# Performance work log

Measured on AMD Instinct MI355X. Metric: run time of the kernel, lower is better.

The kernel has to match this reference:

```python
import jax, jax.numpy as jnp
import numpy as np

D_MODEL, D_LOW, NUM_BINS = 512, 64, 39
DIST_MIN, DIST_MAX = 2.0, 22.0
BIN_WIDTH = (DIST_MAX - DIST_MIN) / (NUM_BINS - 1)
LN_EPS = 1e-5


def setup_inputs() -> dict:
    key = jax.random.key(0)
    ks = jax.random.split(key, 10)
    B, N = 2, 768
    h_res = jax.random.normal(ks[0], (B, N, D_MODEL), dtype=jnp.float32)
    # scale coords so pairwise distances span the [2, 22] bin range
    x_true = jax.random.normal(ks[1], (B, N, 3), dtype=jnp.float32) * 5.0
    token_pad_mask = jnp.ones((B, N), dtype=jnp.float32)
    s = 1.0 / np.sqrt(D_MODEL)
    return {
        "h_res": h_res,
        "x_true": x_true,
        "token_pad_mask": token_pad_mask,
        "ln_w": jnp.ones((D_MODEL,), jnp.float32),
        "ln_b": jnp.zeros((D_MODEL,), jnp.float32),
        "wu_w": jax.random.normal(ks[2], (D_LOW, D_MODEL), jnp.float32) * s,
        "wu_b": jnp.zeros((D_LOW,), jnp.float32),
        "wv_w": jax.random.normal(ks[3], (D_LOW, D_MODEL), jnp.float32) * s,
        "wv_b": jnp.zeros((D_LOW,), jnp.float32),
        "wb_w": jax.random.normal(ks[4], (NUM_BINS, D_LOW), jnp.float32) * (1.0 / np.sqrt(D_LOW)),
        "wb_b": jnp.zeros((NUM_BINS,), jnp.float32),
    }


def _layernorm(x, w, b):
    mu = jnp.mean(x, axis=-1, keepdims=True)
    var = jnp.mean(jnp.square(x - mu), axis=-1, keepdims=True)
    return (x - mu) * jax.lax.rsqrt(var + LN_EPS) * w + b


def reference(h_res, x_true, token_pad_mask, ln_w, ln_b, wu_w, wu_b, wv_w, wv_b, wb_w, wb_b):
    B, N, _ = h_res.shape
    # pairwise distances -> target bins (trunc-to-int then clamp, as torch .long())
    diff = x_true[:, :, None, :] - x_true[:, None, :, :]          # [B,N,N,3]
    d_true = jnp.sqrt(jnp.sum(diff * diff, axis=-1))               # [B,N,N]
    target = jnp.clip(((d_true - DIST_MIN) / BIN_WIDTH).astype(jnp.int32), 0, NUM_BINS - 1)

    h = _layernorm(h_res, ln_w, ln_b)
    U = h @ wu_w.T + wu_b                                          # [B,N,d_low]
    V = h @ wv_w.T + wv_b                                          # [B,N,d_low]
    # logits[b,i,j,k] = sum_c U[b,i,c] V[b,j,c] Wb[k,c] + bb[k]
    logits = jnp.einsum("bic,bjc,kc->bijk", U, V, wb_w) + wb_b     # [B,N,N,K]
    logp = jax.nn.log_softmax(logits, axis=-1)
    ce = -jnp.take_along_axis(logp, target[..., None], axis=-1)[..., 0]  # [B,N,N]

    mask = (token_pad_mask[:, :, None] * token_pad_mask[:, None, :]) > 0  # [B,N,N] bool
    counts = jnp.sum(mask, axis=(1, 2))                            # [B]
    per_sample = jnp.sum(jnp.where(mask, ce, 0.0), axis=(1, 2)) / jnp.maximum(counts, 1)
    valid = counts > 0
    total_count = jnp.sum(valid)
    loss = jnp.sum(jnp.where(valid, per_sample, 0.0)) / jnp.maximum(total_count, 1)
    return loss
```

## Files before the change

### kernel.cpp

```cpp
#include <hip/hip_runtime.h>
#include <hip/hip_bf16.h>
#include <math.h>

#define D_MODEL 512
#define D_LOW   64
#define NBINS   39
#define LOG2E   1.4426950408889634f
#define LN2     0.6931471805599453f

typedef __attribute__((ext_vector_type(8))) short short8;
typedef __attribute__((ext_vector_type(4))) float floatx4;

__global__ __launch_bounds__(256) void lnp_kernel(
    const float* __restrict__ h_res,
    const float* __restrict__ ln_w, const float* __restrict__ ln_b,
    const float* __restrict__ wu_w, const float* __restrict__ wu_b,
    const float* __restrict__ wv_w, const float* __restrict__ wv_b,
    float* __restrict__ U, __hip_bfloat16* __restrict__ Vbf, int N) {
  __shared__ short abuf[16 * 512];
  __shared__ float sred[4][2][16];
  const int tid = threadIdx.x;
  const int wv = tid >> 6, lane = tid & 63;
  const int q = lane >> 4, ln16 = lane & 15;
  const int row0 = blockIdx.x * 16;
  const int og = blockIdx.y;

  float sum = 0.f, ssq = 0.f;
  #pragma unroll
  for (int k2 = 0; k2 < 4; ++k2) {
    const int kc = wv * 4 + k2;
    const float* hp = h_res + (size_t)(row0 + ln16) * D_MODEL + kc * 32 + q * 8;
    const floatx4 x0 = *reinterpret_cast<const floatx4*>(hp);
    const floatx4 x1 = *reinterpret_cast<const floatx4*>(hp + 4);
    short8 a;
    #pragma unroll
    for (int e = 0; e < 4; ++e) {
      sum += x0[e]; ssq += x0[e] * x0[e];
      const __hip_bfloat16 hb = __float2bfloat16(x0[e]);
      a[e] = *reinterpret_cast<const short*>(&hb);
    }
    #pragma unroll
    for (int e = 0; e < 4; ++e) {
      sum += x1[e]; ssq += x1[e] * x1[e];
      const __hip_bfloat16 hb = __float2bfloat16(x1[e]);
      a[4 + e] = *reinterpret_cast<const short*>(&hb);
    }
    *reinterpret_cast<short8*>(&abuf[kc * 512 + q * 128 + ln16 * 8]) = a;
  }
  sum += __shfl_xor(sum, 16); sum += __shfl_xor(sum, 32);
  ssq += __shfl_xor(ssq, 16); ssq += __shfl_xor(ssq, 32);
  if (lane < 16) { sred[wv][0][ln16] = sum; sred[wv][1][ln16] = ssq; }

  const int oloc = wv * 16 + ln16;
  const float scale = og ? 1.0f : LOG2E;
  const float* wrow = (og ? wv_w : wu_w) + (size_t)oloc * D_MODEL;
  short8 bfrag[16];
  float ws = 0.f, sb = 0.f;
  #pragma unroll
  for (int kc = 0; kc < 16; ++kc) {
    const int c0 = kc * 32 + q * 8;
    const floatx4 w0 = *reinterpret_cast<const floatx4*>(wrow + c0);
    const floatx4 w1 = *reinterpret_cast<const floatx4*>(wrow + c0 + 4);
    const floatx4 lw0 = *reinterpret_cast<const floatx4*>(ln_w + c0);
    const floatx4 lw1 = *reinterpret_cast<const floatx4*>(ln_w + c0 + 4);
    const floatx4 lb0 = *reinterpret_cast<const floatx4*>(ln_b + c0);
    const floatx4 lb1 = *reinterpret_cast<const floatx4*>(ln_b + c0 + 4);
    short8 f;
    #pragma unroll
    for (int e = 0; e < 4; ++e) {
      const float t0 = w0[e] * lw0[e] * scale;
      const __hip_bfloat16 h0 = __float2bfloat16(t0);
      f[e] = *reinterpret_cast<const short*>(&h0);
      ws += __bfloat162float(h0);
      sb += w0[e] * lb0[e];

      const float t1 = w1[e] * lw1[e] * scale;
      const __hip_bfloat16 h1 = __float2bfloat16(t1);
      f[4 + e] = *reinterpret_cast<const short*>(&h1);
      ws += __bfloat162float(h1);
      sb += w1[e] * lb1[e];
    }
    bfrag[kc] = f;
  }
  ws += __shfl_xor(ws, 16); ws += __shfl_xor(ws, 32);
  sb += __shfl_xor(sb, 16); sb += __shfl_xor(sb, 32);
  const float bb = scale * ((og ? wv_b[oloc] : wu_b[oloc]) + sb);

  __syncthreads();

  float mu_r[4], rs_r[4];
  #pragma unroll
  for (int r = 0; r < 4; ++r) {
    const int row = q * 4 + r;
    float s = 0.f, s2 = 0.f;
    #pragma unroll
    for (int w = 0; w < 4; ++w) { s += sred[w][0][row]; s2 += sred[w][1][row]; }
    const float mu  = s * (1.0f / (float)D_MODEL);
    const float var = s2 * (1.0f / (float)D_MODEL) - mu * mu;
    mu_r[r] = mu;
    rs_r[r] = rsqrtf(var + 1e-5f);
  }

  floatx4 acc = (floatx4){0.f, 0.f, 0.f, 0.f};
  #pragma unroll
  for (int kc = 0; kc < 16; ++kc) {
    const short8 afr = *reinterpret_cast<const short8*>(
        &abuf[kc * 512 + q * 128 + ln16 * 8]);
    acc = __builtin_amdgcn_mfma_f32_16x16x32_bf16(afr, bfrag[kc], acc, 0, 0, 0);
  }

  #pragma unroll
  for (int r = 0; r < 4; ++r) {
    const int rowg = row0 + q * 4 + r;
    const float val = rs_r[r] * acc[r] - mu_r[r] * rs_r[r] * ws + bb;
    if (og == 0) {
      U[(size_t)rowg * D_LOW + oloc] = val;
    } else {
      Vbf[(size_t)rowg * D_LOW + oloc] = __float2bfloat16(val);
    }
  }
}

__global__ __launch_bounds__(256, 4) void pair_kernel(
    const float* __restrict__ U, const __hip_bfloat16* __restrict__ Vbf,
    const float* __restrict__ wb_w, const float* __restrict__ wb_b,
    const float* __restrict__ x_true, const float* __restrict__ pmask,
    float* __restrict__ part, int N) {
  __shared__ short wsh[6 * 64 * 8];
  __shared__ float rbuf[8];
  const int i    = blockIdx.x;
  const int b    = blockIdx.y >> 2;
  const int qtr  = blockIdx.y & 3;
  const int tid  = threadIdx.x;
  const int wave = tid >> 6, lane = tid & 63;
  const int q = lane >> 4, ln16 = lane & 15;
  const int rowi = b * N + i;
  const int jbase = qtr * (N >> 2) + wave * (N >> 4);
  const int q4 = q * 4;

  const short* Vp = reinterpret_cast<const short*>(Vbf) + (size_t)b * N * D_LOW;
  short8 v[3][2];
  #pragma unroll
  for (int tl = 0; tl < 3; ++tl) {
    const size_t jr = jbase + tl * 16 + ln16;
    v[tl][0] = *reinterpret_cast<const short8*>(Vp + jr * D_LOW + q * 8);
    v[tl][1] = *reinterpret_cast<const short8*>(Vp + jr * D_LOW + 32 + q * 8);
  }

  for (int slot = tid; slot < 384; slot += 256) {
    const int fidx = slot >> 6, l = slot & 63;
    const int t = fidx >> 1, s = fidx & 1;
    const int lq = l >> 4, l16 = l & 15;
    const int n = t * 16 + l16;
    short8 fr = (short8){0, 0, 0, 0, 0, 0, 0, 0};
    if (n < NBINS) {
      const float* up = U + (size_t)rowi * D_LOW + s * 32 + lq * 8;
      const float* wr = wb_w + (size_t)n * D_LOW + s * 32 + lq * 8;
      const floatx4 u0 = *reinterpret_cast<const floatx4*>(up);
      const floatx4 u1 = *reinterpret_cast<const floatx4*>(up + 4);
      const floatx4 w0 = *reinterpret_cast<const floatx4*>(wr);
      const floatx4 w1 = *reinterpret_cast<const floatx4*>(wr + 4);
      #pragma unroll
      for (int e = 0; e < 4; ++e) {
        const __hip_bfloat16 h0 = __float2bfloat16(u0[e] * w0[e]);
        const __hip_bfloat16 h1 = __float2bfloat16(u1[e] * w1[e]);
        fr[e]     = *reinterpret_cast<const short*>(&h0);
        fr[4 + e] = *reinterpret_cast<const short*>(&h1);
      }
    }
    *reinterpret_cast<short8*>(&wsh[slot * 8]) = fr;
  }

  const float xi0 = x_true[rowi * 3 + 0];
  const float xi1 = x_true[rowi * 3 + 1];
  const float xi2 = x_true[rowi * 3 + 2];
  const float pmi = pmask[rowi];
  const float BW  = (22.0f - 2.0f) / 38.0f;
  int tbv[3];
  #pragma unroll
  for (int tl = 0; tl < 3; ++tl) {
    const int rowj = b * N + jbase + tl * 16 + ln16;
    const float dx = xi0 - x_true[rowj * 3 + 0];
    const float dy = xi1 - x_true[rowj * 3 + 1];
    const float dz = xi2 - x_true[rowj * 3 + 2];
    const float d  = sqrtf(dx * dx + dy * dy + dz * dz);
    int tb = (int)((d - 2.0f) / BW);
    tb = tb < 0 ? 0 : (tb > NBINS - 1 ? NBINS - 1 : tb);
    tbv[tl] = (pmi * pmask[rowj] > 0.f) ? tb : -1;
  }

  floatx4 bias_init[3];
  #pragma unroll
  for (int t = 0; t < 3; ++t)
    #pragma unroll
    for (int r = 0; r < 4; ++r) {
      const int bin = t * 16 + q * 4 + r;
      bias_init[t][r] = (bin < NBINS) ? LOG2E * wb_b[bin] : -INFINITY;
    }

  __syncthreads();
  short8 wfrag[3][2];
  #pragma unroll
  for (int t = 0; t < 3; ++t)
    #pragma unroll
    for (int s = 0; s < 2; ++s)
      wfrag[t][s] = *reinterpret_cast<const short8*>(
          &wsh[((t * 2 + s) * 64 + lane) * 8]);

  floatx4 f[3][3];
  #pragma unroll
  for (int tl = 0; tl < 3; ++tl)
    #pragma unroll
    for (int t = 0; t < 3; ++t) {
      floatx4 a = bias_init[t];
      a = __builtin_amdgcn_mfma_f32_16x16x32_bf16(wfrag[t][0], v[tl][0], a, 0, 0, 0);
      a = __builtin_amdgcn_mfma_f32_16x16x32_bf16(wfrag[t][1], v[tl][1], a, 0, 0, 0);
      f[tl][t] = a;
    }

  float sp[3], ltv[3];
  #pragma unroll
  for (int tl = 0; tl < 3; ++tl) {
    const int tbq = tbv[tl] - q4;
    float s0 = 0.f, s1 = 0.f, s2 = 0.f, s3 = 0.f, lt = 0.f;
    #pragma unroll
    for (int t = 0; t < 3; ++t) {
      const floatx4 fv = f[tl][t];
      s0 += __builtin_amdgcn_exp2f(fv[0]);
      s1 += __builtin_amdgcn_exp2f(fv[1]);
      s2 += __builtin_amdgcn_exp2f(fv[2]);
      s3 += __builtin_amdgcn_exp2f(fv[3]);
      lt += (tbq == t * 16 + 0) ? fv[0] : 0.f;
      lt += (tbq == t * 16 + 1) ? fv[1] : 0.f;
      lt += (tbq == t * 16 + 2) ? fv[2] : 0.f;
      lt += (tbq == t * 16 + 3) ? fv[3] : 0.f;
    }
    sp[tl] = (s0 + s1) + (s2 + s3);
    ltv[tl] = lt;
  }

  #pragma unroll
  for (int tl = 0; tl < 3; ++tl) sp[tl] += __shfl_xor(sp[tl], 16);
  #pragma unroll
  for (int tl = 0; tl < 3; ++tl) sp[tl] += __shfl_xor(sp[tl], 32);

  float ce_sum = 0.f, cnt_sum = 0.f;
  #pragma unroll
  for (int tl = 0; tl < 3; ++tl) {
    const float ok = (tbv[tl] >= 0) ? 1.f : 0.f;
    ce_sum  += ok * LN2 * (__builtin_amdgcn_logf(sp[tl]) - 4.0f * ltv[tl]);
    cnt_sum += ok;
  }

  #pragma unroll
  for (int off = 32; off; off >>= 1) {
    ce_sum  += __shfl_xor(ce_sum, off);
    cnt_sum += __shfl_xor(cnt_sum, off);
  }
  if (lane == 0) { rbuf[wave] = ce_sum; rbuf[4 + wave] = cnt_sum; }
  __syncthreads();
  if (tid == 0) {
    const size_t slot = ((size_t)blockIdx.y * N + blockIdx.x) * 2;
    part[slot + 0] = rbuf[0] + rbuf[1] + rbuf[2] + rbuf[3];
    part[slot + 1] = rbuf[4] + rbuf[5] + rbuf[6] + rbuf[7];
  }
}

__global__ __launch_bounds__(256) void finalize_kernel(
    const float* __restrict__ part, float* __restrict__ out, int N, int B) {
  __shared__ float red[8];
  const int tid = threadIdx.x, wave = tid >> 6, lane = tid & 63;
  float loss = 0.f, vcount = 0.f;
  const int nper = 4 * N;
  for (int b = 0; b < B; ++b) {
    float ce = 0.f, cnt = 0.f;
    for (int e = tid; e < nper; e += 256) {
      const size_t base = ((size_t)b * nper + e) * 2;
      ce  += part[base + 0];
      cnt += part[base + 1];
    }
    #pragma unroll
    for (int off = 32; off; off >>= 1) {
      ce  += __shfl_xor(ce, off);
      cnt += __shfl_xor(cnt, off);
    }
    if (lane == 0) { red[wave] = ce; red[4 + wave] = cnt; }
    __syncthreads();
    if (tid == 0) {
      const float s = red[0] + red[1] + red[2] + red[3];
      const float c = red[4] + red[5] + red[6] + red[7];
      if (c > 0.f) { loss += s / fmaxf(c, 1.f); vcount += 1.f; }
    }
    __syncthreads();
  }
  if (tid == 0) out[0] = (vcount > 0.f) ? loss / vcount : 0.f;
}

extern "C" void kernel_launch(void* const* d_in, const int* in_sizes, int n_in,
                              void* d_out, int out_size, void* d_ws, size_t ws_size,
                              hipStream_t stream) {
  const float* h_res  = (const float*)d_in[0];
  const float* x_true = (const float*)d_in[1];
  const float* pmask  = (const float*)d_in[2];
  const float* ln_w   = (const float*)d_in[3];
  const float* ln_b   = (const float*)d_in[4];
  const float* wu_w   = (const float*)d_in[5];
  const float* wu_b   = (const float*)d_in[6];
  const float* wv_w   = (const float*)d_in[7];
  const float* wv_b   = (const float*)d_in[8];
  const float* wb_w   = (const float*)d_in[9];
  const float* wb_b   = (const float*)d_in[10];

  const int B  = 2;
  const int N  = in_sizes[2] / B;
  const int BN = B * N;

  float* U = (float*)d_ws;
  __hip_bfloat16* Vbf = (__hip_bfloat16*)(U + (size_t)BN * D_LOW);
  float* part = (float*)(Vbf + (size_t)BN * D_LOW);

  lnp_kernel<<<dim3(BN / 16, 2), 256, 0, stream>>>(
      h_res, ln_w, ln_b, wu_w, wu_b, wv_w, wv_b, U, Vbf, N);
  pair_kernel<<<dim3(N, 4 * B), 256, 0, stream>>>(
      U, Vbf, wb_w, wb_b, x_true, pmask, part, N);
  finalize_kernel<<<1, 256, 0, stream>>>(part, (float*)d_out, N, B);
}
```

Before: 134.3 us.

## Process four query rows per pair block with 512 threads, reusing V fragments

Reorganizes the pair kernel so each 512-thread block handles four i rows across all N columns (8 waves, 96 columns each) instead of one i row over a quarter of the columns. V fragments loaded into registers are reused across four i rows, and the block count drops from 6144 to 384. The aim is to amortize V loads, weight-fragment setup and launch overhead. In exchange, register pressure rises (6x2 V fragments plus a 4x6 target table), occupancy hints are dropped, and the grid has fewer blocks, which may underfill the GPU.

```diff
diff --git a/kernel.cpp b/kernel.cpp
--- a/kernel.cpp
+++ b/kernel.cpp
@@ -121,41 +121,41 @@
   }
 }
 
-__global__ __launch_bounds__(256, 4) void pair_kernel(
+__global__ __launch_bounds__(512) void pair_kernel(
     const float* __restrict__ U, const __hip_bfloat16* __restrict__ Vbf,
     const float* __restrict__ wb_w, const float* __restrict__ wb_b,
     const float* __restrict__ x_true, const float* __restrict__ pmask,
     float* __restrict__ part, int N) {
-  __shared__ short wsh[6 * 64 * 8];
-  __shared__ float rbuf[8];
-  const int i    = blockIdx.x;
-  const int b    = blockIdx.y >> 2;
-  const int qtr  = blockIdx.y & 3;
-  const int tid  = threadIdx.x;
-  const int wave = tid >> 6, lane = tid & 63;
+  __shared__ short wsh[4 * 6 * 64 * 8];
+  __shared__ float rbuf[16];
+  const int tid = threadIdx.x;
+  const int wv = tid >> 6, lane = tid & 63;
   const int q = lane >> 4, ln16 = lane & 15;
-  const int rowi = b * N + i;
-  const int jbase = qtr * (N >> 2) + wave * (N >> 4);
+  const int i0 = blockIdx.x * 4;
+  const int b  = (i0 >= N) ? 1 : 0;
+  const int jbase = wv * (N >> 3);
   const int q4 = q * 4;
 
   const short* Vp = reinterpret_cast<const short*>(Vbf) + (size_t)b * N * D_LOW;
-  short8 v[3][2];
-  #pragma unroll
-  for (int tl = 0; tl < 3; ++tl) {
+  short8 v[6][2];
+  #pragma unroll
+  for (int tl = 0; tl < 6; ++tl) {
     const size_t jr = jbase + tl * 16 + ln16;
     v[tl][0] = *reinterpret_cast<const short8*>(Vp + jr * D_LOW + q * 8);
     v[tl][1] = *reinterpret_cast<const short8*>(Vp + jr * D_LOW + 32 + q * 8);
   }
 
-  for (int slot = tid; slot < 384; slot += 256) {
-    const int fidx = slot >> 6, l = slot & 63;
-    const int t = fidx >> 1, s = fidx & 1;
+  for (int s = tid; s < 1536; s += 512) {
+    const int ii = s / 384;
+    const int rem = s - ii * 384;
+    const int fidx = rem >> 6, l = rem & 63;
+    const int t = fidx >> 1, ss = fidx & 1;
     const int lq = l >> 4, l16 = l & 15;
     const int n = t * 16 + l16;
     short8 fr = (short8){0, 0, 0, 0, 0, 0, 0, 0};
     if (n < NBINS) {
-      const float* up = U + (size_t)rowi * D_LOW + s * 32 + lq * 8;
-      const float* wr = wb_w + (size_t)n * D_LOW + s * 32 + lq * 8;
+      const float* up = U + (size_t)(i0 + ii) * D_LOW + ss * 32 + lq * 8;
+      const float* wr = wb_w + (size_t)n * D_LOW + ss * 32 + lq * 8;
       const floatx4 u0 = *reinterpret_cast<const floatx4*>(up);
       const floatx4 u1 = *reinterpret_cast<const floatx4*>(up + 4);
       const floatx4 w0 = *reinterpret_cast<const floatx4*>(wr);
@@ -168,25 +168,37 @@
         fr[4 + e] = *reinterpret_cast<const short*>(&h1);
       }
     }
-    *reinterpret_cast<short8*>(&wsh[slot * 8]) = fr;
-  }
-
-  const float xi0 = x_true[rowi * 3 + 0];
-  const float xi1 = x_true[rowi * 3 + 1];
-  const float xi2 = x_true[rowi * 3 + 2];
-  const float pmi = pmask[rowi];
-  const float BW  = (22.0f - 2.0f) / 38.0f;
-  int tbv[3];
-  #pragma unroll
-  for (int tl = 0; tl < 3; ++tl) {
+    *reinterpret_cast<short8*>(&wsh[s * 8]) = fr;
+  }
+
+  float xi0v[4], xi1v[4], xi2v[4], pmiv[4];
+  #pragma unroll
+  for (int ii = 0; ii < 4; ++ii) {
+    const int rowi = i0 + ii;
+    xi0v[ii] = x_true[rowi * 3 + 0];
+    xi1v[ii] = x_true[rowi * 3 + 1];
+    xi2v[ii] = x_true[rowi * 3 + 2];
+    pmiv[ii] = pmask[rowi];
+  }
+  const float BW = (22.0f - 2.0f) / 38.0f;
+  int tb[4][6];
+  #pragma unroll
+  for (int tl = 0; tl < 6; ++tl) {
     const int rowj = b * N + jbase + tl * 16 + ln16;
-    const float dx = xi0 - x_true[rowj * 3 + 0];
-    const float dy = xi1 - x_true[rowj * 3 + 1];
-    const float dz = xi2 - x_true[rowj * 3 + 2];
-    const float d  = sqrtf(dx * dx + dy * dy + dz * dz);
-    int tb = (int)((d - 2.0f) / BW);
-    tb = tb < 0 ? 0 : (tb > NBINS - 1 ? NBINS - 1 : tb);
-    tbv[tl] = (pmi * pmask[rowj] > 0.f) ? tb : -1;
+    const float xj0 = x_true[rowj * 3 + 0];
+    const float xj1 = x_true[rowj * 3 + 1];
+    const float xj2 = x_true[rowj * 3 + 2];
+    const float pmj = pmask[rowj];
+    #pragma unroll
+    for (int ii = 0; ii < 4; ++ii) {
+      const float dx = xi0v[ii] - xj0;
+      const float dy = xi1v[ii] - xj1;
+      const float dz = xi2v[ii] - xj2;
+      const float d  = sqrtf(dx * dx + dy * dy + dz * dz);
+      int t = (int)((d - 2.0f) / BW);
+      t = t < 0 ? 0 : (t > NBINS - 1 ? NBINS - 1 : t);
+      tb[ii][tl] = (pmiv[ii] * pmj > 0.f) ? t : -1;
+    }
   }
 
   floatx4 bias_init[3];
@@ -199,57 +211,50 @@
     }
 
   __syncthreads();
-  short8 wfrag[3][2];
-  #pragma unroll
-  for (int t = 0; t < 3; ++t)
-    #pragma unroll
-    for (int s = 0; s < 2; ++s)
-      wfrag[t][s] = *reinterpret_cast<const short8*>(
-          &wsh[((t * 2 + s) * 64 + lane) * 8]);
-
-  floatx4 f[3][3];
-  #pragma unroll
-  for (int tl = 0; tl < 3; ++tl)
-    #pragma unroll
-    for (int t = 0; t < 3; ++t) {
-      floatx4 a = bias_init[t];
-      a = __builtin_amdgcn_mfma_f32_16x16x32_bf16(wfrag[t][0], v[tl][0], a, 0, 0, 0);
-      a = __builtin_amdgcn_mfma_f32_16x16x32_bf16(wfrag[t][1], v[tl][1], a, 0, 0, 0);
-      f[tl][t] = a;
-    }
-
-  float sp[3], ltv[3];
-  #pragma unroll
-  for (int tl = 0; tl < 3; ++tl) {
-    const int tbq = tbv[tl] - q4;
-    float s0 = 0.f, s1 = 0.f, s2 = 0.f, s3 = 0.f, lt = 0.f;
-    #pragma unroll
-    for (int t = 0; t < 3; ++t) {
-      const floatx4 fv = f[tl][t];
-      s0 += __builtin_amdgcn_exp2f(fv[0]);
-      s1 += __builtin_amdgcn_exp2f(fv[1]);
-      s2 += __builtin_amdgcn_exp2f(fv[2]);
-      s3 += __builtin_amdgcn_exp2f(fv[3]);
-      lt += (tbq == t * 16 + 0) ? fv[0] : 0.f;
-      lt += (tbq == t * 16 + 1) ? fv[1] : 0.f;
-      lt += (tbq == t * 16 + 2) ? fv[2] : 0.f;
-      lt += (tbq == t * 16 + 3) ? fv[3] : 0.f;
-    }
-    sp[tl] = (s0 + s1) + (s2 + s3);
-    ltv[tl] = lt;
-  }
-
-  #pragma unroll
-  for (int tl = 0; tl < 3; ++tl) sp[tl] += __shfl_xor(sp[tl], 16);
-  #pragma unroll
-  for (int tl = 0; tl < 3; ++tl) sp[tl] += __shfl_xor(sp[tl], 32);
 
   float ce_sum = 0.f, cnt_sum = 0.f;
   #pragma unroll
-  for (int tl = 0; tl < 3; ++tl) {
-    const float ok = (tbv[tl] >= 0) ? 1.f : 0.f;
-    ce_sum  += ok * LN2 * (__builtin_amdgcn_logf(sp[tl]) - 4.0f * ltv[tl]);
-    cnt_sum += ok;
+  for (int ii = 0; ii < 4; ++ii) {
+    short8 wfrag[3][2];
+    #pragma unroll
+    for (int t = 0; t < 3; ++t)
+      #pragma unroll
+      for (int s = 0; s < 2; ++s)
+        wfrag[t][s] = *reinterpret_cast<const short8*>(
+            &wsh[((ii * 6 + t * 2 + s) * 64 + lane) * 8]);
+
+    #pragma unroll
+    for (int tl = 0; tl < 6; ++tl) {
+      floatx4 f[3];
+      #pragma unroll
+      for (int t = 0; t < 3; ++t) {
+        floatx4 a = bias_init[t];
+        a = __builtin_amdgcn_mfma_f32_16x16x32_bf16(wfrag[t][0], v[tl][0], a, 0, 0, 0);
+        a = __builtin_amdgcn_mfma_f32_16x16x32_bf16(wfrag[t][1], v[tl][1], a, 0, 0, 0);
+        f[t] = a;
+      }
+
+      const int tbv = tb[ii][tl];
+      const int tbq = tbv - q4;
+      float s0 = 0.f, s1 = 0.f, s2 = 0.f, s3 = 0.f, lt = 0.f;
+      #pragma unroll
+      for (int t = 0; t < 3; ++t) {
+        const floatx4 fv = f[t];
+        s0 += __builtin_amdgcn_exp2f(fv[0]);
+        s1 += __builtin_amdgcn_exp2f(fv[1]);
+        s2 += __builtin_amdgcn_exp2f(fv[2]);
+        s3 += __builtin_amdgcn_exp2f(fv[3]);
+        lt += (tbq == t * 16 + 0) ? fv[0] : 0.f;
+        lt += (tbq == t * 16 + 1) ? fv[1] : 0.f;
+        lt += (tbq == t * 16 + 2) ? fv[2] : 0.f;
+        lt += (tbq == t * 16 + 3) ? fv[3] : 0.f;
+      }
+      float ssum = (s0 + s1) + (s2 + s3);
+      ssum += __shfl_xor(ssum, 16); ssum += __shfl_xor(ssum, 32);
+      const float ok = (tbv >= 0) ? 1.f : 0.f;
+      ce_sum  += ok * LN2 * (__builtin_amdgcn_logf(ssum) - 4.0f * lt);
+      cnt_sum += ok;
+    }
   }
 
   #pragma unroll
@@ -257,12 +262,15 @@
     ce_sum  += __shfl_xor(ce_sum, off);
     cnt_sum += __shfl_xor(cnt_sum, off);
   }
-  if (lane == 0) { rbuf[wave] = ce_sum; rbuf[4 + wave] = cnt_sum; }
+  if (lane == 0) { rbuf[wv] = ce_sum; rbuf[8 + wv] = cnt_sum; }
   __syncthreads();
   if (tid == 0) {
-    const size_t slot = ((size_t)blockIdx.y * N + blockIdx.x) * 2;
-    part[slot + 0] = rbuf[0] + rbuf[1] + rbuf[2] + rbuf[3];
-    part[slot + 1] = rbuf[4] + rbuf[5] + rbuf[6] + rbuf[7];
+    float ce = 0.f, cnt = 0.f;
+    #pragma unroll
+    for (int w = 0; w < 8; ++w) { ce += rbuf[w]; cnt += rbuf[8 + w]; }
+    const size_t slot = (size_t)blockIdx.x * 2;
+    part[slot + 0] = ce;
+    part[slot + 1] = cnt;
   }
 }
 
@@ -271,7 +279,7 @@
   __shared__ float red[8];
   const int tid = threadIdx.x, wave = tid >> 6, lane = tid & 63;
   float loss = 0.f, vcount = 0.f;
-  const int nper = 4 * N;
+  const int nper = N / 4;
   for (int b = 0; b < B; ++b) {
     float ce = 0.f, cnt = 0.f;
     for (int e = tid; e < nper; e += 256) {
@@ -321,7 +329,7 @@
 
   lnp_kernel<<<dim3(BN / 16, 2), 256, 0, stream>>>(
       h_res, ln_w, ln_b, wu_w, wu_b, wv_w, wv_b, U, Vbf, N);
-  pair_kernel<<<dim3(N, 4 * B), 256, 0, stream>>>(
+  pair_kernel<<<BN / 4, 512, 0, stream>>>(
       U, Vbf, wb_w, wb_b, x_true, pmask, part, N);
   finalize_kernel<<<1, 256, 0, stream>>>(part, (float*)d_out, N, B);
 }
```

Result: faster. 121.1 us (-9.8%).
